# Performance work log

Measured on AMD Instinct MI355X. Metric: run time of the kernel, lower is better.

The kernel has to match this reference:

```python
import jax, jax.numpy as jnp
import numpy as np

N_NODES = 100000


def gcn_conv(x, edge_index, W, b):
    """PyG GCNConv: add self-loops, symmetric deg^{-1/2} normalization,
    linear transform, scatter-add aggregation, then bias."""
    n = x.shape[0]
    loops = jnp.arange(n, dtype=edge_index.dtype)
    src = jnp.concatenate([edge_index[0], loops])  # [E+N]
    dst = jnp.concatenate([edge_index[1], loops])  # [E+N]
    # degree (with self-loops) of each target node
    deg = jax.ops.segment_sum(jnp.ones_like(dst, dtype=x.dtype), dst, num_segments=n)
    dinv = jnp.where(deg > 0, jax.lax.rsqrt(deg), 0.0)
    norm = dinv[src] * dinv[dst]  # [E+N]
    h = x @ W  # [N, out_dim] -- transform before aggregation
    msg = h[src] * norm[:, None]  # gather + normalize
    out = jax.ops.segment_sum(msg, dst, num_segments=n)  # scatter-add
    return out + b


def setup_inputs() -> dict:
    key = jax.random.key(0)
    ks = jax.random.split(key, 8)
    n, e, d_in, d_h = N_NODES, 1600000, 32, 64
    x = jax.random.normal(ks[0], (n, d_in), dtype=jnp.float32)
    edge_index = jax.random.randint(ks[1], (2, e), 0, n, dtype=jnp.int64)
    # Glorot-style init for GCN weights, uniform for linear layer
    W1 = jax.random.normal(ks[2], (d_in, d_h), dtype=jnp.float32) / np.sqrt(d_in)
    b1 = jnp.zeros((d_h,), dtype=jnp.float32)
    W2 = jax.random.normal(ks[3], (d_h, d_h), dtype=jnp.float32) / np.sqrt(d_h)
    b2 = jnp.zeros((d_h,), dtype=jnp.float32)
    Wo = jax.random.normal(ks[4], (d_h, 1), dtype=jnp.float32) / np.sqrt(d_h)
    bo = jnp.zeros((1,), dtype=jnp.float32)
    return {"x": x, "edge_index": edge_index, "W1": W1, "b1": b1,
            "W2": W2, "b2": b2, "Wo": Wo, "bo": bo}


def reference(x, edge_index, W1, b1, W2, b2, Wo, bo):
    h = jax.nn.relu(gcn_conv(x, edge_index, W1, b1))
    h = jax.nn.relu(gcn_conv(h, edge_index, W2, b2))
    logits = h @ Wo + bo  # [N, 1]
    return jax.nn.sigmoid(logits).squeeze(-1)  # [N]
```

## Files before the change

kernel.cpp:

```cpp
#include <hip/hip_runtime.h>

#define DH 64
#define DIN 32
#define BSH 8
#define BNODES 256
#define MAXB 1024
#define CAPSH 13
#define CAP (1 << CAPSH)

typedef unsigned short u16;
typedef unsigned int u32;
typedef float f32x2 __attribute__((ext_vector_type(2)));

__device__ __forceinline__ float bf2f(u16 u) {
    union { u32 i; float f; } x; x.i = ((u32)u) << 16; return x.f;
}
__device__ __forceinline__ u16 f2bf(float f) {
    union { float f; u32 i; } x; x.f = f;
    u32 r = x.i + 0x7fff + ((x.i >> 16) & 1);
    return (u16)(r >> 16);
}
__device__ __forceinline__ float bfl(u32 u) {
    union { u32 i; float f; } x; x.i = u << 16; return x.f;
}
__device__ __forceinline__ float bfh(u32 u) {
    union { u32 i; float f; } x; x.i = u & 0xffff0000u; return x.f;
}
__device__ __forceinline__ void pkacc(f32x2& a, u32 u) {
    f32x2 b;
    b[0] = bfl(u); b[1] = bfh(u);
    asm("v_pk_add_f32 %0, %1, %0" : "+v"(a) : "v"(b));
}

__global__ void __launch_bounds__(256) binA_k(
        const int* __restrict__ ei, int* __restrict__ gcnt,
        u32* __restrict__ pairs, int E, int n, int nbuck) {
    __shared__ int lhist[MAXB];
    __shared__ int lbase[MAXB];
    __shared__ int smode;
    int t = threadIdx.x;
    if (t < 64) {
        int v = (2 * t + 1 < 2 * E) ? ei[2 * t + 1] : 0;
        unsigned long long b = __ballot(v != 0);
        if (t == 0) smode = (b != 0ULL) ? 1 : 0;
    }
    for (int b = t; b < nbuck; b += 256) lhist[b] = 0;
    __syncthreads();
    int m = smode;
    unsigned un = (unsigned)n;
    int q0 = blockIdx.x * 256 + t;
    int qs = gridDim.x * 256;

    if (m && !(E & 3)) {
        const int4* d4 = (const int4*)(ei + E);
        for (int q = q0; q < (E >> 2); q += qs) {
            int4 d = d4[q];
            if ((unsigned)d.x < un) atomicAdd(&lhist[d.x >> BSH], 1);
            if ((unsigned)d.y < un) atomicAdd(&lhist[d.y >> BSH], 1);
            if ((unsigned)d.z < un) atomicAdd(&lhist[d.z >> BSH], 1);
            if ((unsigned)d.w < un) atomicAdd(&lhist[d.w >> BSH], 1);
        }
    } else if (!m && !(E & 1)) {
        const int4* d4 = (const int4*)(ei + 2 * E);
        for (int q = q0; q < (E >> 1); q += qs) {
            int4 d = d4[q];
            if ((unsigned)d.x < un) atomicAdd(&lhist[d.x >> BSH], 1);
            if ((unsigned)d.z < un) atomicAdd(&lhist[d.z >> BSH], 1);
        }
    } else {
        const int* dstp = m ? (ei + E) : (ei + 2 * E);
        int stride = m ? 1 : 2;
        for (int e = q0; e < E; e += qs) {
            int d = dstp[(size_t)e * stride];
            if ((unsigned)d < un) atomicAdd(&lhist[d >> BSH], 1);
        }
    }
    __syncthreads();
    for (int b = t; b < nbuck; b += 256) {
        int c = lhist[b];
        lbase[b] = c ? ((b << CAPSH) + atomicAdd(&gcnt[b], c)) : 0;
        lhist[b] = 0;
    }
    __syncthreads();
    #define EMIT(S, D)                                                     \
        if ((unsigned)(D) < un) {                                          \
            int sv = ((unsigned)(S) < un) ? (S) : 0;                       \
            int bb = (D) >> BSH;                                           \
            int off = atomicAdd(&lhist[bb], 1);                            \
            int pos = lbase[bb] + off;                                     \
            if (pos < ((bb + 1) << CAPSH))                                 \
                pairs[pos] = ((u32)sv << BSH) | (u32)((D) & (BNODES - 1)); \
        }
    if (m && !(E & 3)) {
        const int4* s4 = (const int4*)ei;
        const int4* d4 = (const int4*)(ei + E);
        for (int q = q0; q < (E >> 2); q += qs) {
            int4 s = s4[q]; int4 d = d4[q];
            EMIT(s.x, d.x) EMIT(s.y, d.y) EMIT(s.z, d.z) EMIT(s.w, d.w)
        }
    } else if (!m && !(E & 1)) {
        const int4* s4 = (const int4*)ei;
        const int4* d4 = (const int4*)(ei + 2 * E);
        for (int q = q0; q < (E >> 1); q += qs) {
            int4 s = s4[q]; int4 d = d4[q];
            EMIT(s.x, d.x) EMIT(s.z, d.z)
        }
    } else {
        const int* srcp = ei;
        const int* dstp = m ? (ei + E) : (ei + 2 * E);
        int stride = m ? 1 : 2;
        for (int e = q0; e < E; e += qs) {
            int d = dstp[(size_t)e * stride];
            int s = srcp[(size_t)e * stride];
            EMIT(s, d)
        }
    }
    #undef EMIT
}

__global__ void __launch_bounds__(512) csr_gemm_k(
        u32* __restrict__ pairs, const int* __restrict__ gcnt,
        int* __restrict__ rstart, int* __restrict__ rend,
        int* __restrict__ col, float* __restrict__ dinv,
        const float* __restrict__ x, const float* __restrict__ W1, int N) {
    __shared__ int cnt[BNODES];
    __shared__ int s[BNODES];
    __shared__ float dl[BNODES];
    __shared__ float Wl[DIN * DH];
    __shared__ float xl[32][DIN + 4];
    int b = blockIdx.x, t = threadIdx.x;
    int base = b << CAPSH;
    int ec = gcnt[b]; if (ec > CAP) ec = CAP;
    int end = base + ec;
    ((float4*)Wl)[t] = ((const float4*)W1)[t];
    if (t < BNODES) cnt[t] = 0;
    __syncthreads();
    for (int i = base + t; i < end; i += 512)
        atomicAdd(&cnt[pairs[i] & (BNODES - 1)], 1);
    __syncthreads();
    int v = (t < BNODES) ? cnt[t] : 0;
    if (t < BNODES) s[t] = v;
    __syncthreads();
    for (int off = 1; off < BNODES; off <<= 1) {
        int xsc = (t >= off && t < BNODES) ? s[t - off] : 0;
        __syncthreads();
        if (t < BNODES) s[t] += xsc;
        __syncthreads();
    }
    if (t < BNODES) {
        int excl = s[t] - v;
        int a = base + excl;
        int node = (b << BSH) + t;
        float di = rsqrtf((float)v + 1.0f);
        dl[t] = di;
        if (node < N) {
            rstart[node] = a;
            rend[node]   = a + v;
            dinv[node]   = di;
        }
        cnt[t] = a;
    }
    __syncthreads();
    for (int i = base + t; i < end; i += 512) {
        u32 p = pairs[i];
        int pos = atomicAdd(&cnt[p & (BNODES - 1)], 1);
        col[pos] = (int)(p >> BSH);
    }
    __syncthreads();
    u16* hp = (u16*)pairs;
    int lane = t & 63, w = t >> 6;
    int g = lane >> 4, c = lane & 15;
    for (int it = 0; it < 8; it++) {
        int nl0 = it * 32;
        __syncthreads();
        if (t < 256) {
            int idx = t * 4;
            int row = idx / DIN, ck = idx % DIN;
            int node = (b << BSH) + nl0 + row;
            float4 vx = {0.f, 0.f, 0.f, 0.f};
            if (node < N)
                vx = *(const float4*)&x[(size_t)node * DIN + ck];
            *(float4*)&xl[row][ck] = vx;
        }
        __syncthreads();
        int nl = nl0 + w * 4 + g;
        int node = (b << BSH) + nl;
        const float* xr = xl[nl - nl0];
        float4 acc = {0.f, 0.f, 0.f, 0.f};
        #pragma unroll
        for (int k = 0; k < DIN; k++) {
            float xv = xr[k];
            float4 wv = *(const float4*)&Wl[k * DH + c * 4];
            acc.x += xv * wv.x; acc.y += xv * wv.y; acc.z += xv * wv.z; acc.w += xv * wv.w;
        }
        if (node < N) {
            float di = dl[nl];
            ushort4 o;
            o.x = f2bf(acc.x * di); o.y = f2bf(acc.y * di);
            o.z = f2bf(acc.z * di); o.w = f2bf(acc.w * di);
            *(ushort4*)&hp[(size_t)node * DH + c * 4] = o;
        }
    }
    if (b == 0 && t < 32)
        ((float*)((char*)pairs + (size_t)N * DH * 2))[t] = 0.f;
}

__device__ __forceinline__ void edge_sum8(const u16* __restrict__ hp,
                                          const int* __restrict__ col,
                                          int start, int deg, int g, int c,
                                          int nsent, f32x2* __restrict__ acc) {
    int dm = deg;
    dm = max(dm, __shfl_xor(dm, 8, 64));
    dm = max(dm, __shfl_xor(dm, 16, 64));
    dm = max(dm, __shfl_xor(dm, 32, 64));
    if (dm <= 0) return;
    int gl = g << 3;
    u32 co = (u32)c << 4;
    const char* hpb = (const char*)hp;
    int cb = (c < deg) ? col[start + c] : nsent;
    for (int base = 0; base < dm; base += 8) {
        int nb = base + 8;
        int cbn = nsent;
        if (nb < dm) cbn = (nb + c < deg) ? col[start + nb + c] : nsent;
        int s0 = __shfl(cb, gl | 0, 64);
        int s1 = __shfl(cb, gl | 1, 64);
        int s2 = __shfl(cb, gl | 2, 64);
        int s3 = __shfl(cb, gl | 3, 64);
        int s4 = __shfl(cb, gl | 4, 64);
        int s5 = __shfl(cb, gl | 5, 64);
        int s6 = __shfl(cb, gl | 6, 64);
        int s7 = __shfl(cb, gl | 7, 64);
        uint4 v0 = *(const uint4*)(hpb + ((((u32)s0) << 7) | co));
        uint4 v1 = *(const uint4*)(hpb + ((((u32)s1) << 7) | co));
        uint4 v2 = *(const uint4*)(hpb + ((((u32)s2) << 7) | co));
        uint4 v3 = *(const uint4*)(hpb + ((((u32)s3) << 7) | co));
        uint4 v4 = *(const uint4*)(hpb + ((((u32)s4) << 7) | co));
        uint4 v5 = *(const uint4*)(hpb + ((((u32)s5) << 7) | co));
        uint4 v6 = *(const uint4*)(hpb + ((((u32)s6) << 7) | co));
        uint4 v7 = *(const uint4*)(hpb + ((((u32)s7) << 7) | co));
        pkacc(acc[0], v0.x); pkacc(acc[1], v0.y); pkacc(acc[2], v0.z); pkacc(acc[3], v0.w);
        pkacc(acc[0], v1.x); pkacc(acc[1], v1.y); pkacc(acc[2], v1.z); pkacc(acc[3], v1.w);
        pkacc(acc[0], v2.x); pkacc(acc[1], v2.y); pkacc(acc[2], v2.z); pkacc(acc[3], v2.w);
        pkacc(acc[0], v3.x); pkacc(acc[1], v3.y); pkacc(acc[2], v3.z); pkacc(acc[3], v3.w);
        pkacc(acc[0], v4.x); pkacc(acc[1], v4.y); pkacc(acc[2], v4.z); pkacc(acc[3], v4.w);
        pkacc(acc[0], v5.x); pkacc(acc[1], v5.y); pkacc(acc[2], v5.z); pkacc(acc[3], v5.w);
        pkacc(acc[0], v6.x); pkacc(acc[1], v6.y); pkacc(acc[2], v6.z); pkacc(acc[3], v6.w);
        pkacc(acc[0], v7.x); pkacc(acc[1], v7.y); pkacc(acc[2], v7.z); pkacc(acc[3], v7.w);
        cb = cbn;
    }
}

__global__ void __launch_bounds__(256) agg_gemm_k(
        const u16* __restrict__ hp, const int* __restrict__ rstart,
        const int* __restrict__ rend, const int* __restrict__ col,
        const float* __restrict__ dinv, const float* __restrict__ b1,
        const float* __restrict__ W2, u16* __restrict__ hp2, int N) {
    __shared__ float Wl[DH * DH];
    __shared__ float xs[4][8][DH + 4];
    int tid = threadIdx.x;
    {
        const float4* Wv = (const float4*)W2;
        float4* Wd = (float4*)Wl;
        #pragma unroll
        for (int r = 0; r < 4; r++) Wd[tid + 256 * r] = Wv[tid + 256 * r];
    }
    if (blockIdx.x == 0 && tid < 32)
        ((float*)(hp2 + (size_t)N * DH))[tid] = 0.f;
    __syncthreads();
    int lane = tid & 63, w = tid >> 6;
    int g = lane >> 3, c = lane & 7;
    int node = blockIdx.x * 32 + w * 8 + g;
    int start = 0, deg = 0;
    if (node < N) { start = rstart[node]; deg = rend[node] - start; }
    f32x2 acc[4] = {{0.f,0.f},{0.f,0.f},{0.f,0.f},{0.f,0.f}};
    edge_sum8(hp, col, start, deg, g, c, N, acc);
    float di = (node < N) ? dinv[node] : 0.f;
    float o0=0.f,o1=0.f,o2=0.f,o3=0.f,o4=0.f,o5=0.f,o6=0.f,o7=0.f;
    if (node < N) {
        uint4 sv = *(const uint4*)&hp[(size_t)node * DH + c * 8];
        float4 blo = *(const float4*)&b1[c * 8];
        float4 bhi = *(const float4*)&b1[c * 8 + 4];
        o0 = fmaxf((acc[0][0] + bfl(sv.x)) * di + blo.x, 0.f);
        o1 = fmaxf((acc[0][1] + bfh(sv.x)) * di + blo.y, 0.f);
        o2 = fmaxf((acc[1][0] + bfl(sv.y)) * di + blo.z, 0.f);
        o3 = fmaxf((acc[1][1] + bfh(sv.y)) * di + blo.w, 0.f);
        o4 = fmaxf((acc[2][0] + bfl(sv.z)) * di + bhi.x, 0.f);
        o5 = fmaxf((acc[2][1] + bfh(sv.z)) * di + bhi.y, 0.f);
        o6 = fmaxf((acc[3][0] + bfl(sv.w)) * di + bhi.z, 0.f);
        o7 = fmaxf((acc[3][1] + bfh(sv.w)) * di + bhi.w, 0.f);
    }
    *(float4*)&xs[w][g][c * 8]     = make_float4(o0, o1, o2, o3);
    *(float4*)&xs[w][g][c * 8 + 4] = make_float4(o4, o5, o6, o7);
    const float* xr = xs[w][g];
    float4 alo = {0.f,0.f,0.f,0.f}, ahi = {0.f,0.f,0.f,0.f};
    #pragma unroll
    for (int k4 = 0; k4 < DH / 4; k4++) {
        float4 xv4 = *(const float4*)&xr[k4 * 4];
        float xj[4] = {xv4.x, xv4.y, xv4.z, xv4.w};
        #pragma unroll
        for (int j = 0; j < 4; j++) {
            const float* wr = &Wl[(k4 * 4 + j) * DH + c * 8];
            float4 w0 = *(const float4*)wr;
            float4 w1 = *(const float4*)(wr + 4);
            float xv = xj[j];
            alo.x += xv * w0.x; alo.y += xv * w0.y; alo.z += xv * w0.z; alo.w += xv * w0.w;
            ahi.x += xv * w1.x; ahi.y += xv * w1.y; ahi.z += xv * w1.z; ahi.w += xv * w1.w;
        }
    }
    if (node < N) {
        uint4 po;
        po.x = (u32)f2bf(alo.x * di) | ((u32)f2bf(alo.y * di) << 16);
        po.y = (u32)f2bf(alo.z * di) | ((u32)f2bf(alo.w * di) << 16);
        po.z = (u32)f2bf(ahi.x * di) | ((u32)f2bf(ahi.y * di) << 16);
        po.w = (u32)f2bf(ahi.z * di) | ((u32)f2bf(ahi.w * di) << 16);
        *(uint4*)&hp2[(size_t)node * DH + c * 8] = po;
    }
}

__global__ void __launch_bounds__(256) agg_head_k(
        const u16* __restrict__ hp, const int* __restrict__ rstart,
        const int* __restrict__ rend, const int* __restrict__ col,
        const float* __restrict__ dinv, const float* __restrict__ bias,
        const float* __restrict__ Wo, const float* __restrict__ bo,
        float* __restrict__ y, int N) {
    int lane = threadIdx.x & 63;
    int g = lane >> 3, c = lane & 7;
    int node = blockIdx.x * 32 + (threadIdx.x >> 6) * 8 + g;
    int start = 0, deg = 0;
    if (node < N) { start = rstart[node]; deg = rend[node] - start; }
    f32x2 acc[4] = {{0.f,0.f},{0.f,0.f},{0.f,0.f},{0.f,0.f}};
    edge_sum8(hp, col, start, deg, g, c, N, acc);
    float t = 0.f;
    if (node < N) {
        uint4 sv = *(const uint4*)&hp[(size_t)node * DH + c * 8];
        float4 blo = *(const float4*)&bias[c * 8];
        float4 bhi = *(const float4*)&bias[c * 8 + 4];
        float4 wlo = *(const float4*)&Wo[c * 8];
        float4 whi = *(const float4*)&Wo[c * 8 + 4];
        float di = dinv[node];
        t = fmaxf((acc[0][0] + bfl(sv.x)) * di + blo.x, 0.f) * wlo.x
          + fmaxf((acc[0][1] + bfh(sv.x)) * di + blo.y, 0.f) * wlo.y
          + fmaxf((acc[1][0] + bfl(sv.y)) * di + blo.z, 0.f) * wlo.z
          + fmaxf((acc[1][1] + bfh(sv.y)) * di + blo.w, 0.f) * wlo.w
          + fmaxf((acc[2][0] + bfl(sv.z)) * di + bhi.x, 0.f) * whi.x
          + fmaxf((acc[2][1] + bfh(sv.z)) * di + bhi.y, 0.f) * whi.y
          + fmaxf((acc[3][0] + bfl(sv.w)) * di + bhi.z, 0.f) * whi.z
          + fmaxf((acc[3][1] + bfh(sv.w)) * di + bhi.w, 0.f) * whi.w;
    }
    t += __shfl_xor(t, 1, 64);
    t += __shfl_xor(t, 2, 64);
    t += __shfl_xor(t, 4, 64);
    if (c == 0 && node < N) {
        float z = t + bo[0];
        y[node] = 1.f / (1.f + __expf(-z));
    }
}

extern "C" void kernel_launch(void* const* d_in, const int* in_sizes, int n_in,
                              void* d_out, int out_size, void* d_ws, size_t ws_size,
                              hipStream_t stream) {
    const float* x  = (const float*)d_in[0];
    const int*   ei = (const int*)d_in[1];
    const float* W1 = (const float*)d_in[2];
    const float* b1 = (const float*)d_in[3];
    const float* W2 = (const float*)d_in[4];
    const float* b2 = (const float*)d_in[5];
    const float* Wo = (const float*)d_in[6];
    const float* bo = (const float*)d_in[7];
    float* y = (float*)d_out;

    int N = in_sizes[0] / DIN;
    int E = in_sizes[1] / 2;
    int nbuck = ((N - 1) >> BSH) + 1;

    char* ws = (char*)d_ws;
    size_t off = 0;
    auto alloc = [&](size_t bytes) { char* p = ws + off; off += (bytes + 255) & ~(size_t)255; return p; };
    int*   gcnt   = (int*)alloc(MAXB * 4);
    int*   rstart = (int*)alloc((size_t)N * 4);
    int*   rend   = (int*)alloc((size_t)N * 4);
    float* dinv   = (float*)alloc((size_t)N * 4);
    int*   col    = (int*)alloc(((size_t)nbuck << CAPSH) * 4);
    size_t pair_b = ((size_t)nbuck << CAPSH) * 4;
    size_t hp_b   = (size_t)N * DH * 2 + 256;
    char*  bufA   = (char*)alloc(pair_b > hp_b ? pair_b : hp_b);
    u16*   bufB   = (u16*)alloc(hp_b);
    u16*   hp    = (u16*)bufA;
    u32*   pairs = (u32*)bufA;

    int gN32 = (N + 31) / 32;

    hipMemsetAsync(gcnt, 0, (size_t)nbuck * 4, stream);
    binA_k<<<768, 256, 0, stream>>>(ei, gcnt, pairs, E, N, nbuck);
    csr_gemm_k<<<nbuck, 512, 0, stream>>>(pairs, gcnt, rstart, rend, col, dinv, x, W1, N);
    agg_gemm_k<<<gN32, 256, 0, stream>>>(hp, rstart, rend, col, dinv, b1, W2, bufB, N);
    agg_head_k<<<gN32, 256, 0, stream>>>(bufB, rstart, rend, col, dinv, b2, Wo, bo, y, N);
}
```

Baseline: 199.0 us.

## Split CSR build from first GEMM, double-buffer edge gathers, enlarge aggregation blocks

Splits the fused CSR-build-plus-GEMM kernel into a CSR build kernel and a separate, widely parallel GEMM1 kernel over 16-node blocks, so the first transform is no longer serialized within 391 bucket blocks. Adds a double-buffered edge gather in the head aggregation that issues the next 8 neighbor loads before accumulating the current ones, giving more memory-level parallelism at the cost of extra registers. Also moves agg_gemm_k to 512-thread blocks covering 64 nodes. The extra launch and the re-read of dinv from global memory add some overhead.

```diff
diff --git a/kernel.cpp b/kernel.cpp
--- a/kernel.cpp
+++ b/kernel.cpp
@@ -118,21 +118,16 @@
     #undef EMIT
 }
 
-__global__ void __launch_bounds__(512) csr_gemm_k(
-        u32* __restrict__ pairs, const int* __restrict__ gcnt,
+__global__ void __launch_bounds__(512) csr_build_k(
+        const u32* __restrict__ pairs, const int* __restrict__ gcnt,
         int* __restrict__ rstart, int* __restrict__ rend,
-        int* __restrict__ col, float* __restrict__ dinv,
-        const float* __restrict__ x, const float* __restrict__ W1, int N) {
+        int* __restrict__ col, float* __restrict__ dinv, int N) {
     __shared__ int cnt[BNODES];
     __shared__ int s[BNODES];
-    __shared__ float dl[BNODES];
-    __shared__ float Wl[DIN * DH];
-    __shared__ float xl[32][DIN + 4];
     int b = blockIdx.x, t = threadIdx.x;
     int base = b << CAPSH;
     int ec = gcnt[b]; if (ec > CAP) ec = CAP;
     int end = base + ec;
-    ((float4*)Wl)[t] = ((const float4*)W1)[t];
     if (t < BNODES) cnt[t] = 0;
     __syncthreads();
     for (int i = base + t; i < end; i += 512)
@@ -151,12 +146,10 @@
         int excl = s[t] - v;
         int a = base + excl;
         int node = (b << BSH) + t;
-        float di = rsqrtf((float)v + 1.0f);
-        dl[t] = di;
         if (node < N) {
             rstart[node] = a;
             rend[node]   = a + v;
-            dinv[node]   = di;
+            dinv[node]   = rsqrtf((float)v + 1.0f);
         }
         cnt[t] = a;
     }
@@ -166,43 +159,50 @@
         int pos = atomicAdd(&cnt[p & (BNODES - 1)], 1);
         col[pos] = (int)(p >> BSH);
     }
-    __syncthreads();
-    u16* hp = (u16*)pairs;
+}
+
+__global__ void __launch_bounds__(256) gemm1_k(
+        const float* __restrict__ x, const float* __restrict__ W1,
+        const float* __restrict__ dinv, u16* __restrict__ hp, int N) {
+    __shared__ float Wl[DIN * DH];
+    __shared__ float xl[16][DIN + 4];
+    int t = threadIdx.x;
+    {
+        const float4* Wv = (const float4*)W1;
+        float4* Wd = (float4*)Wl;
+        #pragma unroll
+        for (int r = 0; r < 2; r++) Wd[t + 256 * r] = Wv[t + 256 * r];
+    }
+    if (blockIdx.x == 0 && t < 32)
+        ((float*)(hp + (size_t)N * DH))[t] = 0.f;
+    if (t < 128) {
+        int row = t >> 3, ck = (t & 7) * 4;
+        int node = blockIdx.x * 16 + row;
+        float4 vx = {0.f, 0.f, 0.f, 0.f};
+        if (node < N)
+            vx = *(const float4*)&x[(size_t)node * DIN + ck];
+        *(float4*)&xl[row][ck] = vx;
+    }
+    __syncthreads();
     int lane = t & 63, w = t >> 6;
     int g = lane >> 4, c = lane & 15;
-    for (int it = 0; it < 8; it++) {
-        int nl0 = it * 32;
-        __syncthreads();
-        if (t < 256) {
-            int idx = t * 4;
-            int row = idx / DIN, ck = idx % DIN;
-            int node = (b << BSH) + nl0 + row;
-            float4 vx = {0.f, 0.f, 0.f, 0.f};
-            if (node < N)
-                vx = *(const float4*)&x[(size_t)node * DIN + ck];
-            *(float4*)&xl[row][ck] = vx;
-        }
-        __syncthreads();
-        int nl = nl0 + w * 4 + g;
-        int node = (b << BSH) + nl;
-        const float* xr = xl[nl - nl0];
-        float4 acc = {0.f, 0.f, 0.f, 0.f};
-        #pragma unroll
-        for (int k = 0; k < DIN; k++) {
-            float xv = xr[k];
-            float4 wv = *(const float4*)&Wl[k * DH + c * 4];
-            acc.x += xv * wv.x; acc.y += xv * wv.y; acc.z += xv * wv.z; acc.w += xv * wv.w;
-        }
-        if (node < N) {
-            float di = dl[nl];
-            ushort4 o;
-            o.x = f2bf(acc.x * di); o.y = f2bf(acc.y * di);
-            o.z = f2bf(acc.z * di); o.w = f2bf(acc.w * di);
-            *(ushort4*)&hp[(size_t)node * DH + c * 4] = o;
-        }
-    }
-    if (b == 0 && t < 32)
-        ((float*)((char*)pairs + (size_t)N * DH * 2))[t] = 0.f;
+    int nl = w * 4 + g;
+    int node = blockIdx.x * 16 + nl;
+    const float* xr = xl[nl];
+    float4 acc = {0.f, 0.f, 0.f, 0.f};
+    #pragma unroll
+    for (int k = 0; k < DIN; k++) {
+        float xv = xr[k];
+        float4 wv = *(const float4*)&Wl[k * DH + c * 4];
+        acc.x += xv * wv.x; acc.y += xv * wv.y; acc.z += xv * wv.z; acc.w += xv * wv.w;
+    }
+    if (node < N) {
+        float di = dinv[node];
+        ushort4 o;
+        o.x = f2bf(acc.x * di); o.y = f2bf(acc.y * di);
+        o.z = f2bf(acc.z * di); o.w = f2bf(acc.w * di);
+        *(ushort4*)&hp[(size_t)node * DH + c * 4] = o;
+    }
 }
 
 __device__ __forceinline__ void edge_sum8(const u16* __restrict__ hp,
@@ -250,26 +250,66 @@
     }
 }
 
-__global__ void __launch_bounds__(256) agg_gemm_k(
+__device__ __forceinline__ void edge_sum8_db(const u16* __restrict__ hp,
+                                             const int* __restrict__ col,
+                                             int start, int deg, int g, int c,
+                                             int nsent, f32x2* __restrict__ acc) {
+    int dm = deg;
+    dm = max(dm, __shfl_xor(dm, 8, 64));
+    dm = max(dm, __shfl_xor(dm, 16, 64));
+    dm = max(dm, __shfl_xor(dm, 32, 64));
+    if (dm <= 0) return;
+    int gl = g << 3;
+    u32 co = (u32)c << 4;
+    const char* hpb = (const char*)hp;
+    #define COLS(B) (((B) < dm && (B) + c < deg) ? col[start + (B) + c] : nsent)
+    #define ISSUE(V, CB)                                                     \
+        { _Pragma("unroll") for (int j = 0; j < 8; j++) {                    \
+              int s_ = __shfl((CB), gl | j, 64);                             \
+              (V)[j] = *(const uint4*)(hpb + ((((u32)s_) << 7) | co)); } }
+    #define ACCUM(V)                                                         \
+        { _Pragma("unroll") for (int j = 0; j < 8; j++) {                    \
+              pkacc(acc[0], (V)[j].x); pkacc(acc[1], (V)[j].y);              \
+              pkacc(acc[2], (V)[j].z); pkacc(acc[3], (V)[j].w); } }
+    uint4 va[8], vb[8];
+    int cbA = COLS(0);
+    ISSUE(va, cbA)
+    int cbB = COLS(8);
+    for (int base = 0; base < dm; base += 16) {
+        bool hb = base + 8 < dm;
+        if (hb) ISSUE(vb, cbB)
+        int cbN1 = COLS(base + 16);
+        ACCUM(va)
+        if (base + 16 < dm) ISSUE(va, cbN1)
+        int cbN2 = COLS(base + 24);
+        if (hb) ACCUM(vb)
+        cbB = cbN2;
+    }
+    #undef COLS
+    #undef ISSUE
+    #undef ACCUM
+}
+
+__global__ void __launch_bounds__(512, 8) agg_gemm_k(
         const u16* __restrict__ hp, const int* __restrict__ rstart,
         const int* __restrict__ rend, const int* __restrict__ col,
         const float* __restrict__ dinv, const float* __restrict__ b1,
         const float* __restrict__ W2, u16* __restrict__ hp2, int N) {
     __shared__ float Wl[DH * DH];
-    __shared__ float xs[4][8][DH + 4];
+    __shared__ float xs[8][8][DH + 4];
     int tid = threadIdx.x;
     {
         const float4* Wv = (const float4*)W2;
         float4* Wd = (float4*)Wl;
         #pragma unroll
-        for (int r = 0; r < 4; r++) Wd[tid + 256 * r] = Wv[tid + 256 * r];
+        for (int r = 0; r < 2; r++) Wd[tid + 512 * r] = Wv[tid + 512 * r];
     }
     if (blockIdx.x == 0 && tid < 32)
         ((float*)(hp2 + (size_t)N * DH))[tid] = 0.f;
     __syncthreads();
     int lane = tid & 63, w = tid >> 6;
     int g = lane >> 3, c = lane & 7;
-    int node = blockIdx.x * 32 + w * 8 + g;
+    int node = blockIdx.x * 64 + w * 8 + g;
     int start = 0, deg = 0;
     if (node < N) { start = rstart[node]; deg = rend[node] - start; }
     f32x2 acc[4] = {{0.f,0.f},{0.f,0.f},{0.f,0.f},{0.f,0.f}};
@@ -329,7 +369,7 @@
     int start = 0, deg = 0;
     if (node < N) { start = rstart[node]; deg = rend[node] - start; }
     f32x2 acc[4] = {{0.f,0.f},{0.f,0.f},{0.f,0.f},{0.f,0.f}};
-    edge_sum8(hp, col, start, deg, g, c, N, acc);
+    edge_sum8_db(hp, col, start, deg, g, c, N, acc);
     float t = 0.f;
     if (node < N) {
         uint4 sv = *(const uint4*)&hp[(size_t)node * DH + c * 8];
@@ -388,11 +428,10 @@
     u16*   hp    = (u16*)bufA;
     u32*   pairs = (u32*)bufA;
 
-    int gN32 = (N + 31) / 32;
-
     hipMemsetAsync(gcnt, 0, (size_t)nbuck * 4, stream);
     binA_k<<<768, 256, 0, stream>>>(ei, gcnt, pairs, E, N, nbuck);
-    csr_gemm_k<<<nbuck, 512, 0, stream>>>(pairs, gcnt, rstart, rend, col, dinv, x, W1, N);
-    agg_gemm_k<<<gN32, 256, 0, stream>>>(hp, rstart, rend, col, dinv, b1, W2, bufB, N);
-    agg_head_k<<<gN32, 256, 0, stream>>>(bufB, rstart, rend, col, dinv, b2, Wo, bo, y, N);
-}
+    csr_build_k<<<nbuck, 512, 0, stream>>>(pairs, gcnt, rstart, rend, col, dinv, N);
+    gemm1_k<<<(N + 15) / 16, 256, 0, stream>>>(x, W1, dinv, hp, N);
+    agg_gemm_k<<<(N + 63) / 64, 512, 0, stream>>>(hp, rstart, rend, col, dinv, b1, W2, bufB, N);
+    agg_head_k<<<(N + 31) / 32, 256, 0, stream>>>(bufB, rstart, rend, col, dinv, b2, Wo, bo, y, N);
+}
```

After: 201.5 us. Within noise of the previous version (+1.3%).
